# Performance work log

Hardware: AMD Instinct MI355X
Metric: run time of the kernel (lower is better)

## Reference

```python
import jax, jax.numpy as jnp
import numpy as np

B, S, HID = 2, 2048, 5120
H = 32
D_NOPE, D_ROPE, D_V = 128, 64, 128
D_Q = D_NOPE + D_ROPE          # 192, q/k head dim
Q_RANK, KV_RANK = 1536, 512
THETA = 10000.0
EPS = 1e-6


def setup_inputs() -> dict:
    key = jax.random.key(0)
    ks = jax.random.split(key, 8)
    w = lambda k, shape: jax.random.normal(k, shape, jnp.float32) * 0.02
    hidden_states = jax.random.normal(ks[0], (B, S, HID), jnp.float32)
    position_ids = jnp.broadcast_to(jnp.arange(S, dtype=jnp.int32), (B, S))
    attention_mask = jnp.broadcast_to(
        jnp.tril(jnp.ones((S, S), bool))[None, None], (B, 1, S, S))
    return {
        "hidden_states": hidden_states,
        "q_a_proj_w": w(ks[1], (Q_RANK, HID)),
        "q_a_ln_w": jnp.ones((Q_RANK,), jnp.float32),
        "q_b_proj_w": w(ks[2], (H * D_Q, Q_RANK)),
        "kv_a_proj_w": w(ks[3], (KV_RANK + D_ROPE, HID)),
        "kv_a_ln_w": jnp.ones((KV_RANK,), jnp.float32),
        "kv_b_proj_w": w(ks[4], (H * (D_NOPE + D_V), KV_RANK)),
        "o_proj_w": w(ks[5], (HID, H * D_V)),
        "position_ids": position_ids,
        "attention_mask": attention_mask,
    }


def _rms_norm(x, w, eps=EPS):
    x32 = x.astype(jnp.float32)
    var = jnp.mean(x32 * x32, axis=-1, keepdims=True)
    return (x32 * jax.lax.rsqrt(var + eps)).astype(x.dtype) * w


def _deinterleave(x):
    # view(..., d//2, 2).transpose(-1, -2).reshape(..., d)
    return jnp.concatenate([x[..., 0::2], x[..., 1::2]], axis=-1)


def _rotate_half(x):
    h = x.shape[-1] // 2
    return jnp.concatenate([-x[..., h:], x[..., :h]], axis=-1)


def _mla_forward(hidden_states, q_a_proj_w, q_a_ln_w, q_b_proj_w,
                 kv_a_proj_w, kv_a_ln_w, kv_b_proj_w, o_proj_w,
                 position_ids, attention_mask):
    b, s, _ = hidden_states.shape
    # low-rank Q path
    q_c = hidden_states @ q_a_proj_w.T                        # [b,s,Q_RANK]
    q = _rms_norm(q_c, q_a_ln_w) @ q_b_proj_w.T               # [b,s,H*D_Q]
    q = q.reshape(b, s, H, D_Q).transpose(0, 2, 1, 3)         # [b,H,s,D_Q]
    q_nope, q_pe = q[..., :D_NOPE], q[..., D_NOPE:]
    # compressed KV path (MQA rope part shared across heads)
    ckv = hidden_states @ kv_a_proj_w.T                       # [b,s,KV_RANK+D_ROPE]
    compressed, k_pe = ckv[..., :KV_RANK], ckv[..., KV_RANK:]
    k_pe = k_pe.reshape(b, s, 1, D_ROPE).transpose(0, 2, 1, 3)  # [b,1,s,D_ROPE]
    kv = _rms_norm(compressed, kv_a_ln_w) @ kv_b_proj_w.T     # [b,s,H*(D_NOPE+D_V)]
    kv = kv.reshape(b, s, H, D_NOPE + D_V).transpose(0, 2, 1, 3)
    k_nope, v = kv[..., :D_NOPE], kv[..., D_NOPE:]
    # decoupled RoPE (interleaved layout, DeepSeek-V2 style)
    inv_freq = 1.0 / (THETA ** (jnp.arange(0, D_ROPE, 2, dtype=jnp.float32) / D_ROPE))
    t = jnp.arange(s, dtype=jnp.float32)
    emb = jnp.concatenate([t[:, None] * inv_freq, t[:, None] * inv_freq], axis=-1)
    cos = jnp.cos(emb)[position_ids][:, None]                 # [b,1,s,D_ROPE]
    sin = jnp.sin(emb)[position_ids][:, None]
    q_pe = _deinterleave(q_pe)
    k_pe = _deinterleave(k_pe)
    q_pe = q_pe * cos + _rotate_half(q_pe) * sin
    k_pe = k_pe * cos + _rotate_half(k_pe) * sin
    # assemble full q/k and attend
    query = jnp.concatenate([q_nope, q_pe], axis=-1)          # [b,H,s,D_Q]
    key = jnp.concatenate(
        [k_nope, jnp.broadcast_to(k_pe, (b, H, s, D_ROPE))], axis=-1)
    scale = D_Q ** -0.5
    scores = jnp.einsum('bhqd,bhkd->bhqk', query, key) * scale
    scores = jnp.where(attention_mask, scores, jnp.float32(-1e9))
    probs = jax.nn.softmax(scores.astype(jnp.float32), axis=-1).astype(query.dtype)
    attn = jnp.einsum('bhqk,bhkd->bhqd', probs, v)            # [b,H,s,D_V]
    attn = attn.transpose(0, 2, 1, 3).reshape(b, s, H * D_V)
    return attn @ o_proj_w.T                                   # [b,s,HID]


def reference(hidden_states, q_a_proj_w, q_a_ln_w, q_b_proj_w,
              kv_a_proj_w, kv_a_ln_w, kv_b_proj_w, o_proj_w,
              position_ids, attention_mask):
    return _mla_forward(hidden_states, q_a_proj_w, q_a_ln_w, q_b_proj_w,
                        kv_a_proj_w, kv_a_ln_w, kv_b_proj_w, o_proj_w,
                        position_ids, attention_mask)
```

## Files before the change

### kernel.cpp

```cpp
#include <hip/hip_runtime.h>
#include <hip/hip_bf16.h>

typedef __bf16 bf16_t;
typedef __bf16 bf16x4 __attribute__((ext_vector_type(4)));
typedef __bf16 bf16x8 __attribute__((ext_vector_type(8)));
typedef float f32x4 __attribute__((ext_vector_type(4)));

#define B_ 2
#define S_ 2048
#define HID_ 5120
#define H_ 32
#define D_NOPE_ 128
#define D_ROPE_ 64
#define D_V_ 128
#define D_Q_ 192
#define EPS_ 1e-6f

#define GLDS16(g, l)                                                          \
  __builtin_amdgcn_global_load_lds(                                           \
      (const __attribute__((address_space(1))) void*)(g),                     \
      (__attribute__((address_space(3))) void*)(l), 16, 0, 0)

__global__ __launch_bounds__(256) void f32_to_bf16_k(const float* __restrict__ x,
                                                     bf16_t* __restrict__ y, long n) {
  long i = ((long)blockIdx.x * 256 + threadIdx.x) * 8;
  if (i + 8 <= n) {
    float4 f0 = *(const float4*)(x + i);
    float4 f1 = *(const float4*)(x + i + 4);
    bf16x8 o;
    o[0] = (bf16_t)f0.x; o[1] = (bf16_t)f0.y; o[2] = (bf16_t)f0.z; o[3] = (bf16_t)f0.w;
    o[4] = (bf16_t)f1.x; o[5] = (bf16_t)f1.y; o[6] = (bf16_t)f1.z; o[7] = (bf16_t)f1.w;
    *(bf16x8*)(y + i) = o;
  }
}

template <int CMODE>
__global__ __launch_bounds__(256) void gemm128(const bf16_t* __restrict__ A,
                                               const bf16_t* __restrict__ W,
                                               void* __restrict__ Cv,
                                               bf16_t* __restrict__ vTp,
                                               int M, int N, int K) {
  __shared__ bf16_t As[128 * 32];
  __shared__ bf16_t Ws[128 * 32];
  const int tid = threadIdx.x;
  const int lane = tid & 63;
  const int wave = tid >> 6;
  const int bm = blockIdx.y * 128;
  const int bn = blockIdx.x * 128;
  const int wm = (wave >> 1) * 64;
  const int wn = (wave & 1) * 64;
  const int ll = lane & 15;
  const int kg = (lane >> 4) * 8;
  const int r0 = tid >> 2;
  const int cc0 = (tid & 3) * 8;
  const bf16_t* Ag0 = A + (size_t)(bm + r0) * K + cc0;
  const bf16_t* Ag1 = A + (size_t)(bm + 64 + r0) * K + cc0;
  const bf16_t* Wg0 = W + (size_t)(bn + r0) * K + cc0;
  const bf16_t* Wg1 = W + (size_t)(bn + 64 + r0) * K + cc0;
  bf16_t* Al0 = &As[tid * 8];
  bf16_t* Al1 = &As[(tid + 256) * 8];
  bf16_t* Wl0 = &Ws[tid * 8];
  bf16_t* Wl1 = &Ws[(tid + 256) * 8];

  f32x4 acc[4][4];
#pragma unroll
  for (int m = 0; m < 4; m++)
#pragma unroll
    for (int n = 0; n < 4; n++) acc[m][n] = {};

  for (int k0 = 0; k0 < K; k0 += 32) {
    GLDS16(Ag0 + k0, Al0);
    GLDS16(Ag1 + k0, Al1);
    GLDS16(Wg0 + k0, Wl0);
    GLDS16(Wg1 + k0, Wl1);
    __syncthreads();
    bf16x8 af[4], bfr[4];
#pragma unroll
    for (int m = 0; m < 4; m++)
      af[m] = *(const bf16x8*)&As[(wm + m * 16 + ll) * 32 + kg];
#pragma unroll
    for (int n = 0; n < 4; n++)
      bfr[n] = *(const bf16x8*)&Ws[(wn + n * 16 + ll) * 32 + kg];
#pragma unroll
    for (int m = 0; m < 4; m++)
#pragma unroll
      for (int n = 0; n < 4; n++)
        acc[m][n] = __builtin_amdgcn_mfma_f32_16x16x32_bf16(af[m], bfr[n], acc[m][n], 0, 0, 0);
    __syncthreads();
  }

  const int rb = (lane >> 4) * 4;
  if constexpr (CMODE == 2) {
    bf16_t* KN = (bf16_t*)Cv;
#pragma unroll
    for (int m = 0; m < 4; m++)
#pragma unroll
      for (int n = 0; n < 4; n++) {
        int mrow = bm + wm + m * 16 + rb;
        int nn = bn + wn + n * 16 + ll;
        int hh = nn >> 8, cc = nn & 255;
        if (cc < 128) {
          bf16_t* p = KN + ((size_t)mrow * H_ + hh) * 128 + cc;
#pragma unroll
          for (int rr = 0; rr < 4; rr++)
            p[(size_t)rr * (H_ * 128)] = (bf16_t)acc[m][n][rr];
        } else {
          int bb = mrow >> 11;
          int s0 = mrow & 2047;
          bf16x4 o;
          o[0] = (bf16_t)acc[m][n][0]; o[1] = (bf16_t)acc[m][n][1];
          o[2] = (bf16_t)acc[m][n][2]; o[3] = (bf16_t)acc[m][n][3];
          *(bf16x4*)(vTp + (((size_t)bb * H_ + hh) * 128 + (cc - 128)) * S_ + s0) = o;
        }
      }
  } else {
#pragma unroll
    for (int m = 0; m < 4; m++)
#pragma unroll
      for (int n = 0; n < 4; n++) {
        int row = bm + wm + m * 16 + rb;
        int col = bn + wn + n * 16 + ll;
        if (CMODE == 1) {
          float* C = (float*)Cv;
#pragma unroll
          for (int rr = 0; rr < 4; rr++)
            C[(size_t)(row + rr) * N + col] = acc[m][n][rr];
        } else {
          bf16_t* C = (bf16_t*)Cv;
#pragma unroll
          for (int rr = 0; rr < 4; rr++)
            C[(size_t)(row + rr) * N + col] = (bf16_t)acc[m][n][rr];
        }
      }
  }
}

__global__ __launch_bounds__(256) void gemm_bt64(const bf16_t* __restrict__ A,
                                                 const bf16_t* __restrict__ W,
                                                 bf16_t* __restrict__ C,
                                                 int M, int N, int K) {
  __shared__ bf16_t As[64 * 40];
  __shared__ bf16_t Ws[64 * 40];
  const int tid = threadIdx.x;
  const int bm = blockIdx.y * 64;
  const int bn = blockIdx.x * 64;
  const int wave = tid >> 6, lane = tid & 63;
  const int wm = (wave >> 1) * 32, wn = (wave & 1) * 32;
  const int srow = tid >> 2;
  const int scol = (tid & 3) * 8;
  const bf16_t* Ap16 = A + (size_t)(bm + srow) * K + scol;
  const bf16_t* Wp = W + (size_t)(bn + srow) * K + scol;
  f32x4 acc00 = {}, acc01 = {}, acc10 = {}, acc11 = {};
  const int r = lane & 15;
  const int kq = (lane >> 4) * 8;
  for (int k0 = 0; k0 < K; k0 += 32) {
    *(bf16x8*)&As[srow * 40 + scol] = *(const bf16x8*)(Ap16 + k0);
    *(bf16x8*)&Ws[srow * 40 + scol] = *(const bf16x8*)(Wp + k0);
    __syncthreads();
    bf16x8 a0 = *(bf16x8*)&As[(wm + r) * 40 + kq];
    bf16x8 a1 = *(bf16x8*)&As[(wm + 16 + r) * 40 + kq];
    bf16x8 b0 = *(bf16x8*)&Ws[(wn + r) * 40 + kq];
    bf16x8 b1 = *(bf16x8*)&Ws[(wn + 16 + r) * 40 + kq];
    acc00 = __builtin_amdgcn_mfma_f32_16x16x32_bf16(a0, b0, acc00, 0, 0, 0);
    acc01 = __builtin_amdgcn_mfma_f32_16x16x32_bf16(a0, b1, acc01, 0, 0, 0);
    acc10 = __builtin_amdgcn_mfma_f32_16x16x32_bf16(a1, b0, acc10, 0, 0, 0);
    acc11 = __builtin_amdgcn_mfma_f32_16x16x32_bf16(a1, b1, acc11, 0, 0, 0);
    __syncthreads();
  }
  const int col = lane & 15;
  const int rb = (lane >> 4) * 4;
#pragma unroll
  for (int rr = 0; rr < 4; rr++) {
    int m0r = bm + wm + rb + rr;
    int m1r = m0r + 16;
    C[(size_t)m0r * N + (bn + wn + col)]      = (bf16_t)acc00[rr];
    C[(size_t)m0r * N + (bn + wn + 16 + col)] = (bf16_t)acc01[rr];
    C[(size_t)m1r * N + (bn + wn + col)]      = (bf16_t)acc10[rr];
    C[(size_t)m1r * N + (bn + wn + 16 + col)] = (bf16_t)acc11[rr];
  }
}

__global__ __launch_bounds__(256) void rmsnorm_k(const bf16_t* __restrict__ x,
                                                 const float* __restrict__ w,
                                                 bf16_t* __restrict__ y,
                                                 int dim, int xstride) {
  const int row = blockIdx.x;
  const bf16_t* xr = x + (size_t)row * xstride;
  bf16_t* yr = y + (size_t)row * dim;
  float ss = 0.f;
  for (int i = threadIdx.x; i < dim; i += 256) {
    float v = (float)xr[i];
    ss += v * v;
  }
  for (int off = 32; off > 0; off >>= 1) ss += __shfl_down(ss, off);
  __shared__ float red[4];
  __shared__ float s_rinv;
  if ((threadIdx.x & 63) == 0) red[threadIdx.x >> 6] = ss;
  __syncthreads();
  if (threadIdx.x == 0) {
    float tot = red[0] + red[1] + red[2] + red[3];
    s_rinv = 1.0f / sqrtf(tot / (float)dim + EPS_);
  }
  __syncthreads();
  float rinv = s_rinv;
  for (int i = threadIdx.x; i < dim; i += 256)
    yr[i] = (bf16_t)((float)xr[i] * rinv * w[i]);
}

__global__ __launch_bounds__(64) void rope_k(const bf16_t* __restrict__ src,
                                             bf16_t* __restrict__ dst,
                                             const int* __restrict__ pos_ids,
                                             int heads_per_pos, int sstride,
                                             int dstride) {
  __shared__ float xs[64];
  const int rrow = blockIdx.x;
  const int j = threadIdx.x;
  const bf16_t* s = src + (size_t)rrow * sstride;
  xs[j] = (float)s[j];
  __syncthreads();
  const int pos = pos_ids[rrow / heads_per_pos];
  const int i = j & 31;
  float freq = powf(10000.0f, -(float)i / 32.0f);
  float ang = (float)pos * freq;
  float c = cosf(ang), sn = sinf(ang);
  float outv;
  if (j < 32)
    outv = xs[2 * j] * c - xs[2 * j + 1] * sn;
  else
    outv = xs[2 * i + 1] * c + xs[2 * i] * sn;
  dst[(size_t)rrow * dstride + j] = (bf16_t)outv;
}

__global__ __launch_bounds__(256, 2) void flash_attn2(
    const bf16_t* __restrict__ q, const bf16_t* __restrict__ knope,
    const bf16_t* __restrict__ kpe, const bf16_t* __restrict__ vT,
    bf16_t* __restrict__ attn) {
  __shared__ bf16_t KF[12288];
  __shared__ bf16_t VF[8192];
  __shared__ bf16_t PF[8192];
  const int tid = threadIdx.x;
  const int w = tid >> 6;
  const int lane = tid & 63;
  const int ll = lane & 15;
  const int g0 = lane >> 4;
  const int bh = blockIdx.y;
  const int b = bh >> 5;
  const int h = bh & 31;
  const int q0 = ((int)gridDim.x - 1 - (int)blockIdx.x) * 128;
  const int bS = b * S_;
  bf16_t* PFw = PF + w * 2048;

  bf16x8 qf[2][6];
#pragma unroll
  for (int qs = 0; qs < 2; qs++)
#pragma unroll
    for (int ks = 0; ks < 6; ks++)
      qf[qs][ks] = *(const bf16x8*)(
          q + (((size_t)(bS + q0 + 32 * w + 16 * qs + ll)) * H_ + h) * D_Q_ +
          32 * ks + 8 * g0);

  f32x4 acc[2][8];
#pragma unroll
  for (int qs = 0; qs < 2; qs++)
#pragma unroll
    for (int dt = 0; dt < 8; dt++) acc[qs][dt] = {};
  float m_run[2] = {-1e30f, -1e30f};
  float l_run[2] = {0.f, 0.f};

  const bf16_t* kptr[6];
  int kstr[6];
#pragma unroll
  for (int i = 0; i < 6; i++) {
    int c = tid + 256 * i;
    int t_ = c / 384;
    int rem = c - t_ * 384;
    int ks_ = rem >> 6;
    int g_ = (rem >> 4) & 3;
    int ll_ = c & 15;
    int row = 16 * t_ + ll_;
    int k = 32 * ks_ + 8 * g_;
    if (k < 128) {
      kptr[i] = knope + ((size_t)(bS + row) * H_ + h) * 128 + k;
      kstr[i] = H_ * 128;
    } else {
      kptr[i] = kpe + (size_t)(bS + row) * 64 + (k - 128);
      kstr[i] = 64;
    }
  }
  const bf16_t* vptr[4];
#pragma unroll
  for (int i = 0; i < 4; i++) {
    int c = tid + 256 * i;
    int ll_ = c & 15;
    int g_ = (c >> 4) & 3;
    int ks2_ = (c >> 6) & 1;
    int dt_ = c >> 7;
    vptr[i] = vT + (((size_t)b * H_ + h) * 128 + 16 * dt_ + ll_) * S_ +
              32 * ks2_ + 8 * g_;
  }

  bf16x8 kst[6], vst[4];
  auto load_kv = [&]() {
#pragma unroll
    for (int i = 0; i < 6; i++) kst[i] = *(const bf16x8*)kptr[i];
#pragma unroll
    for (int i = 0; i < 4; i++) vst[i] = *(const bf16x8*)vptr[i];
#pragma unroll
    for (int i = 0; i < 6; i++) kptr[i] += (size_t)64 * kstr[i];
#pragma unroll
    for (int i = 0; i < 4; i++) vptr[i] += 64;
  };

  load_kv();
  const int nkt = (q0 >> 6) + 2;
  const float scale = 0.07216878364870322f;

  for (int kt = 0; kt < nkt; kt++) {
    const int k0 = kt * 64;
    __syncthreads();
#pragma unroll
    for (int i = 0; i < 6; i++) *(bf16x8*)&KF[(tid + 256 * i) * 8] = kst[i];
#pragma unroll
    for (int i = 0; i < 4; i++) *(bf16x8*)&VF[(tid + 256 * i) * 8] = vst[i];
    __syncthreads();
    if (kt + 1 < nkt) load_kv();

    f32x4 sv[2][4];
#pragma unroll
    for (int qs = 0; qs < 2; qs++)
#pragma unroll
      for (int t = 0; t < 4; t++) sv[qs][t] = {};
#pragma unroll
    for (int ks = 0; ks < 6; ks++) {
      bf16x8 bq0 = qf[0][ks], bq1 = qf[1][ks];
#pragma unroll
      for (int t = 0; t < 4; t++) {
        bf16x8 ak = *(bf16x8*)&KF[(t * 6 + ks) * 512 + lane * 8];
        sv[0][t] = __builtin_amdgcn_mfma_f32_16x16x32_bf16(ak, bq0, sv[0][t], 0, 0, 0);
        sv[1][t] = __builtin_amdgcn_mfma_f32_16x16x32_bf16(ak, bq1, sv[1][t], 0, 0, 0);
      }
    }

    float alq[2];
#pragma unroll
    for (int qs = 0; qs < 2; qs++) {
      const int qg = q0 + 32 * w + 16 * qs + ll;
      float mx = m_run[qs];
#pragma unroll
      for (int t = 0; t < 4; t++)
#pragma unroll
        for (int r = 0; r < 4; r++) {
          float s = sv[qs][t][r] * scale;
          int kv = k0 + 16 * t + 4 * g0 + r;
          s = (kv > qg) ? -1e30f : s;
          sv[qs][t][r] = s;
          mx = fmaxf(mx, s);
        }
      mx = fmaxf(mx, __shfl_xor(mx, 16));
      mx = fmaxf(mx, __shfl_xor(mx, 32));
      float al = __expf(m_run[qs] - mx);
      float rs = 0.f;
#pragma unroll
      for (int t = 0; t < 4; t++) {
        bf16x4 pv;
#pragma unroll
        for (int r = 0; r < 4; r++) {
          float p = __expf(sv[qs][t][r] - mx);
          rs += p;
          pv[r] = (bf16_t)p;
        }
        int elem = ((qs * 2 + (t >> 1)) * 4 + 2 * (t & 1) + (g0 >> 1)) * 128 +
                   ll * 8 + 4 * (g0 & 1);
        *(bf16x4*)&PFw[elem] = pv;
      }
      rs += __shfl_xor(rs, 16);
      rs += __shfl_xor(rs, 32);
      l_run[qs] = l_run[qs] * al + rs;
      m_run[qs] = mx;
      alq[qs] = al;
    }

#pragma unroll
    for (int qs = 0; qs < 2; qs++)
#pragma unroll
      for (int r = 0; r < 4; r++) {
        float a = __shfl(alq[qs], 4 * g0 + r);
#pragma unroll
        for (int dt = 0; dt < 8; dt++) acc[qs][dt][r] *= a;
      }

#pragma unroll
    for (int ks2 = 0; ks2 < 2; ks2++) {
      bf16x8 ap0 = *(bf16x8*)&PFw[ks2 * 512 + lane * 8];
      bf16x8 ap1 = *(bf16x8*)&PFw[(2 + ks2) * 512 + lane * 8];
#pragma unroll
      for (int dt = 0; dt < 8; dt++) {
        bf16x8 bv = *(bf16x8*)&VF[(dt * 2 + ks2) * 512 + lane * 8];
        acc[0][dt] = __builtin_amdgcn_mfma_f32_16x16x32_bf16(ap0, bv, acc[0][dt], 0, 0, 0);
        acc[1][dt] = __builtin_amdgcn_mfma_f32_16x16x32_bf16(ap1, bv, acc[1][dt], 0, 0, 0);
      }
    }
  }

#pragma unroll
  for (int qs = 0; qs < 2; qs++) {
    float linv = 1.f / l_run[qs];
#pragma unroll
    for (int r = 0; r < 4; r++) {
      float inv = __shfl(linv, 4 * g0 + r);
      int qrow = q0 + 32 * w + 16 * qs + 4 * g0 + r;
      bf16_t* op = attn + (((size_t)(bS + qrow)) * H_ + h) * D_V_ + ll;
#pragma unroll
      for (int dt = 0; dt < 8; dt++)
        op[dt * 16] = (bf16_t)(acc[qs][dt][r] * inv);
    }
  }
}

extern "C" void kernel_launch(void* const* d_in, const int* in_sizes, int n_in,
                              void* d_out, int out_size, void* d_ws, size_t ws_size,
                              hipStream_t stream) {
  const float* hidden  = (const float*)d_in[0];
  const float* q_a_w   = (const float*)d_in[1];
  const float* q_a_ln  = (const float*)d_in[2];
  const float* q_b_w   = (const float*)d_in[3];
  const float* kv_a_w  = (const float*)d_in[4];
  const float* kv_a_ln = (const float*)d_in[5];
  const float* kv_b_w  = (const float*)d_in[6];
  const float* o_w     = (const float*)d_in[7];
  const int*   pos_ids = (const int*)d_in[8];
  float* out = (float*)d_out;
  char* ws = (char*)d_ws;
  const int M = B_ * S_;

  bf16_t* q_ws   = (bf16_t*)(ws + 0);
  bf16_t* knope_ws=(bf16_t*)(ws + 50331648);
  bf16_t* vT_ws  = (bf16_t*)(ws + 83886080);
  bf16_t* kpe_ws = (bf16_t*)(ws + 117440512);
  bf16_t* Wslot  = (bf16_t*)(ws + 117964800);
  bf16_t* qc_ws  = (bf16_t*)(ws + 159907840);
  bf16_t* qcn_ws = (bf16_t*)(ws + 172490752);
  bf16_t* ckv_ws = (bf16_t*)(ws + 185073664);
  bf16_t* ckvn_ws= (bf16_t*)(ws + 189792256);
  bf16_t* attn_ws= (bf16_t*)(ws + 159907840);
  bf16_t* hid_bf = (bf16_t*)(ws + 50331648);

  f32_to_bf16_k<<<(int)((4096L * 5120) / 2048), 256, 0, stream>>>(hidden, hid_bf, 4096L * 5120);
  f32_to_bf16_k<<<1536 * 5120 / 2048, 256, 0, stream>>>(q_a_w, Wslot, 1536L * 5120);
  gemm128<0><<<dim3(1536 / 128, M / 128), 256, 0, stream>>>(hid_bf, Wslot, qc_ws, nullptr, M, 1536, 5120);
  rmsnorm_k<<<M, 256, 0, stream>>>(qc_ws, q_a_ln, qcn_ws, 1536, 1536);
  f32_to_bf16_k<<<576 * 5120 / 2048, 256, 0, stream>>>(kv_a_w, Wslot, 576L * 5120);
  gemm_bt64<<<dim3(576 / 64, M / 64), 256, 0, stream>>>(hid_bf, Wslot, ckv_ws, M, 576, 5120);
  rmsnorm_k<<<M, 256, 0, stream>>>(ckv_ws, kv_a_ln, ckvn_ws, 512, 576);
  f32_to_bf16_k<<<6144 * 1536 / 2048, 256, 0, stream>>>(q_b_w, Wslot, 6144L * 1536);
  gemm128<0><<<dim3(6144 / 128, M / 128), 256, 0, stream>>>(qcn_ws, Wslot, q_ws, nullptr, M, 6144, 1536);
  f32_to_bf16_k<<<8192 * 512 / 2048, 256, 0, stream>>>(kv_b_w, Wslot, 8192L * 512);
  gemm128<2><<<dim3(8192 / 128, M / 128), 256, 0, stream>>>(ckvn_ws, Wslot, knope_ws, vT_ws, M, 8192, 512);
  rope_k<<<M * H_, 64, 0, stream>>>(q_ws + 128, q_ws + 128, pos_ids, H_, D_Q_, D_Q_);
  rope_k<<<M, 64, 0, stream>>>(ckv_ws + 512, kpe_ws, pos_ids, 1, 576, 64);
  flash_attn2<<<dim3(S_ / 128, B_ * H_), 256, 0, stream>>>(q_ws, knope_ws, kpe_ws, vT_ws, attn_ws);
  f32_to_bf16_k<<<5120 * 4096 / 2048, 256, 0, stream>>>(o_w, Wslot, 5120L * 4096);
  gemm128<1><<<dim3(5120 / 128, M / 128), 256, 0, stream>>>(attn_ws, Wslot, out, nullptr, M, 5120, 4096);
}
```

Baseline: 1.281 ms.

## Restructure flash attention to 512 threads with one 16-row Q tile per wave

The attention kernel moves from 4 waves each handling 32 query rows to 8 waves each handling 16 rows. This halves per-wave register state (accumulators, Q fragments, staging) to raise occupancy and spreads the K/V loads over more threads. It also folds the softmax scale and log2e into Q so exp2 can be used, skips the causal mask on tiles that are fully below the diagonal, and raises wave priority around the MFMA loops. The rope kernel swaps powf/cosf/sinf for exp2f and the fast __sincosf, which trades some accuracy at large angles for cheaper math. Rounding the pre-scaled Q to bf16 adds a little extra rounding error.

```diff
diff --git a/kernel.cpp b/kernel.cpp
--- a/kernel.cpp
+++ b/kernel.cpp
@@ -220,9 +220,10 @@
   __syncthreads();
   const int pos = pos_ids[rrow / heads_per_pos];
   const int i = j & 31;
-  float freq = powf(10000.0f, -(float)i / 32.0f);
+  float freq = exp2f(-(float)i * 0.4152410118609203f);
   float ang = (float)pos * freq;
-  float c = cosf(ang), sn = sinf(ang);
+  float c, sn;
+  __sincosf(ang, &sn, &c);
   float outv;
   if (j < 32)
     outv = xs[2 * j] * c - xs[2 * j + 1] * sn;
@@ -231,7 +232,7 @@
   dst[(size_t)rrow * dstride + j] = (bf16_t)outv;
 }
 
-__global__ __launch_bounds__(256, 2) void flash_attn2(
+__global__ __launch_bounds__(512, 4) void flash_attn3(
     const bf16_t* __restrict__ q, const bf16_t* __restrict__ knope,
     const bf16_t* __restrict__ kpe, const bf16_t* __restrict__ vT,
     bf16_t* __restrict__ attn) {
@@ -248,30 +249,30 @@
   const int h = bh & 31;
   const int q0 = ((int)gridDim.x - 1 - (int)blockIdx.x) * 128;
   const int bS = b * S_;
-  bf16_t* PFw = PF + w * 2048;
-
-  bf16x8 qf[2][6];
-#pragma unroll
-  for (int qs = 0; qs < 2; qs++)
-#pragma unroll
-    for (int ks = 0; ks < 6; ks++)
-      qf[qs][ks] = *(const bf16x8*)(
-          q + (((size_t)(bS + q0 + 32 * w + 16 * qs + ll)) * H_ + h) * D_Q_ +
-          32 * ks + 8 * g0);
-
-  f32x4 acc[2][8];
-#pragma unroll
-  for (int qs = 0; qs < 2; qs++)
-#pragma unroll
-    for (int dt = 0; dt < 8; dt++) acc[qs][dt] = {};
-  float m_run[2] = {-1e30f, -1e30f};
-  float l_run[2] = {0.f, 0.f};
-
-  const bf16_t* kptr[6];
-  int kstr[6];
-#pragma unroll
-  for (int i = 0; i < 6; i++) {
-    int c = tid + 256 * i;
+  bf16_t* PFw = PF + w * 1024;
+
+  const float qsc = 0.07216878364870322f * 1.4426950408889634f;
+  bf16x8 qf[6];
+#pragma unroll
+  for (int ks = 0; ks < 6; ks++) {
+    bf16x8 raw = *(const bf16x8*)(
+        q + (((size_t)(bS + q0 + 16 * w + ll)) * H_ + h) * D_Q_ + 32 * ks + 8 * g0);
+    bf16x8 sc;
+#pragma unroll
+    for (int j = 0; j < 8; j++) sc[j] = (bf16_t)((float)raw[j] * qsc);
+    qf[ks] = sc;
+  }
+
+  f32x4 acc[8];
+#pragma unroll
+  for (int dt = 0; dt < 8; dt++) acc[dt] = {};
+  float m_run = -1e30f, l_run = 0.f;
+
+  const bf16_t* kptr[3];
+  int kstr[3];
+#pragma unroll
+  for (int i = 0; i < 3; i++) {
+    int c = tid + 512 * i;
     int t_ = c / 384;
     int rem = c - t_ * 384;
     int ks_ = rem >> 6;
@@ -287,10 +288,10 @@
       kstr[i] = 64;
     }
   }
-  const bf16_t* vptr[4];
-#pragma unroll
-  for (int i = 0; i < 4; i++) {
-    int c = tid + 256 * i;
+  const bf16_t* vptr[2];
+#pragma unroll
+  for (int i = 0; i < 2; i++) {
+    int c = tid + 512 * i;
     int ll_ = c & 15;
     int g_ = (c >> 4) & 3;
     int ks2_ = (c >> 6) & 1;
@@ -299,121 +300,114 @@
               32 * ks2_ + 8 * g_;
   }
 
-  bf16x8 kst[6], vst[4];
+  bf16x8 kst[3], vst[2];
   auto load_kv = [&]() {
 #pragma unroll
-    for (int i = 0; i < 6; i++) kst[i] = *(const bf16x8*)kptr[i];
-#pragma unroll
-    for (int i = 0; i < 4; i++) vst[i] = *(const bf16x8*)vptr[i];
-#pragma unroll
-    for (int i = 0; i < 6; i++) kptr[i] += (size_t)64 * kstr[i];
-#pragma unroll
-    for (int i = 0; i < 4; i++) vptr[i] += 64;
+    for (int i = 0; i < 3; i++) kst[i] = *(const bf16x8*)kptr[i];
+#pragma unroll
+    for (int i = 0; i < 2; i++) vst[i] = *(const bf16x8*)vptr[i];
+#pragma unroll
+    for (int i = 0; i < 3; i++) kptr[i] += (size_t)64 * kstr[i];
+#pragma unroll
+    for (int i = 0; i < 2; i++) vptr[i] += 64;
   };
 
   load_kv();
   const int nkt = (q0 >> 6) + 2;
-  const float scale = 0.07216878364870322f;
 
   for (int kt = 0; kt < nkt; kt++) {
     const int k0 = kt * 64;
     __syncthreads();
 #pragma unroll
-    for (int i = 0; i < 6; i++) *(bf16x8*)&KF[(tid + 256 * i) * 8] = kst[i];
-#pragma unroll
-    for (int i = 0; i < 4; i++) *(bf16x8*)&VF[(tid + 256 * i) * 8] = vst[i];
+    for (int i = 0; i < 3; i++) *(bf16x8*)&KF[(tid + 512 * i) * 8] = kst[i];
+#pragma unroll
+    for (int i = 0; i < 2; i++) *(bf16x8*)&VF[(tid + 512 * i) * 8] = vst[i];
     __syncthreads();
     if (kt + 1 < nkt) load_kv();
 
-    f32x4 sv[2][4];
-#pragma unroll
-    for (int qs = 0; qs < 2; qs++)
-#pragma unroll
-      for (int t = 0; t < 4; t++) sv[qs][t] = {};
+    f32x4 sv[4];
+#pragma unroll
+    for (int t = 0; t < 4; t++) sv[t] = {};
+    __builtin_amdgcn_s_setprio(1);
 #pragma unroll
     for (int ks = 0; ks < 6; ks++) {
-      bf16x8 bq0 = qf[0][ks], bq1 = qf[1][ks];
+      bf16x8 bq = qf[ks];
 #pragma unroll
       for (int t = 0; t < 4; t++) {
         bf16x8 ak = *(bf16x8*)&KF[(t * 6 + ks) * 512 + lane * 8];
-        sv[0][t] = __builtin_amdgcn_mfma_f32_16x16x32_bf16(ak, bq0, sv[0][t], 0, 0, 0);
-        sv[1][t] = __builtin_amdgcn_mfma_f32_16x16x32_bf16(ak, bq1, sv[1][t], 0, 0, 0);
+        sv[t] = __builtin_amdgcn_mfma_f32_16x16x32_bf16(ak, bq, sv[t], 0, 0, 0);
       }
     }
-
-    float alq[2];
-#pragma unroll
-    for (int qs = 0; qs < 2; qs++) {
-      const int qg = q0 + 32 * w + 16 * qs + ll;
-      float mx = m_run[qs];
+    __builtin_amdgcn_s_setprio(0);
+
+    const int qg = q0 + 16 * w + ll;
+    float mx = m_run;
+    if (k0 + 63 > q0 + 16 * w) {
 #pragma unroll
       for (int t = 0; t < 4; t++)
 #pragma unroll
         for (int r = 0; r < 4; r++) {
-          float s = sv[qs][t][r] * scale;
-          int kv = k0 + 16 * t + 4 * g0 + r;
-          s = (kv > qg) ? -1e30f : s;
-          sv[qs][t][r] = s;
+          float s = sv[t][r];
+          s = (k0 + 16 * t + 4 * g0 + r > qg) ? -1e30f : s;
+          sv[t][r] = s;
           mx = fmaxf(mx, s);
         }
-      mx = fmaxf(mx, __shfl_xor(mx, 16));
-      mx = fmaxf(mx, __shfl_xor(mx, 32));
-      float al = __expf(m_run[qs] - mx);
-      float rs = 0.f;
-#pragma unroll
-      for (int t = 0; t < 4; t++) {
-        bf16x4 pv;
-#pragma unroll
-        for (int r = 0; r < 4; r++) {
-          float p = __expf(sv[qs][t][r] - mx);
-          rs += p;
-          pv[r] = (bf16_t)p;
-        }
-        int elem = ((qs * 2 + (t >> 1)) * 4 + 2 * (t & 1) + (g0 >> 1)) * 128 +
-                   ll * 8 + 4 * (g0 & 1);
-        *(bf16x4*)&PFw[elem] = pv;
+    } else {
+#pragma unroll
+      for (int t = 0; t < 4; t++)
+#pragma unroll
+        for (int r = 0; r < 4; r++) mx = fmaxf(mx, sv[t][r]);
+    }
+    mx = fmaxf(mx, __shfl_xor(mx, 16));
+    mx = fmaxf(mx, __shfl_xor(mx, 32));
+    float al = exp2f(m_run - mx);
+    float rs = 0.f;
+#pragma unroll
+    for (int t = 0; t < 4; t++) {
+      bf16x4 pv;
+#pragma unroll
+      for (int r = 0; r < 4; r++) {
+        float p = exp2f(sv[t][r] - mx);
+        rs += p;
+        pv[r] = (bf16_t)p;
       }
-      rs += __shfl_xor(rs, 16);
-      rs += __shfl_xor(rs, 32);
-      l_run[qs] = l_run[qs] * al + rs;
-      m_run[qs] = mx;
-      alq[qs] = al;
-    }
-
-#pragma unroll
-    for (int qs = 0; qs < 2; qs++)
-#pragma unroll
-      for (int r = 0; r < 4; r++) {
-        float a = __shfl(alq[qs], 4 * g0 + r);
-#pragma unroll
-        for (int dt = 0; dt < 8; dt++) acc[qs][dt][r] *= a;
-      }
-
+      int elem = ((t >> 1) * 4 + 2 * (t & 1) + (g0 >> 1)) * 128 + ll * 8 + 4 * (g0 & 1);
+      *(bf16x4*)&PFw[elem] = pv;
+    }
+    rs += __shfl_xor(rs, 16);
+    rs += __shfl_xor(rs, 32);
+    l_run = l_run * al + rs;
+    m_run = mx;
+
+#pragma unroll
+    for (int r = 0; r < 4; r++) {
+      float a = __shfl(al, 4 * g0 + r);
+#pragma unroll
+      for (int dt = 0; dt < 8; dt++) acc[dt][r] *= a;
+    }
+
+    __builtin_amdgcn_s_setprio(1);
 #pragma unroll
     for (int ks2 = 0; ks2 < 2; ks2++) {
-      bf16x8 ap0 = *(bf16x8*)&PFw[ks2 * 512 + lane * 8];
-      bf16x8 ap1 = *(bf16x8*)&PFw[(2 + ks2) * 512 + lane * 8];
+      bf16x8 ap = *(bf16x8*)&PFw[ks2 * 512 + lane * 8];
 #pragma unroll
       for (int dt = 0; dt < 8; dt++) {
         bf16x8 bv = *(bf16x8*)&VF[(dt * 2 + ks2) * 512 + lane * 8];
-        acc[0][dt] = __builtin_amdgcn_mfma_f32_16x16x32_bf16(ap0, bv, acc[0][dt], 0, 0, 0);
-        acc[1][dt] = __builtin_amdgcn_mfma_f32_16x16x32_bf16(ap1, bv, acc[1][dt], 0, 0, 0);
+        acc[dt] = __builtin_amdgcn_mfma_f32_16x16x32_bf16(ap, bv, acc[dt], 0, 0, 0);
       }
     }
-  }
-
-#pragma unroll
-  for (int qs = 0; qs < 2; qs++) {
-    float linv = 1.f / l_run[qs];
-#pragma unroll
-    for (int r = 0; r < 4; r++) {
-      float inv = __shfl(linv, 4 * g0 + r);
-      int qrow = q0 + 32 * w + 16 * qs + 4 * g0 + r;
-      bf16_t* op = attn + (((size_t)(bS + qrow)) * H_ + h) * D_V_ + ll;
-#pragma unroll
-      for (int dt = 0; dt < 8; dt++)
-        op[dt * 16] = (bf16_t)(acc[qs][dt][r] * inv);
-    }
+    __builtin_amdgcn_s_setprio(0);
+  }
+
+  float linv = 1.f / l_run;
+#pragma unroll
+  for (int r = 0; r < 4; r++) {
+    float inv = __shfl(linv, 4 * g0 + r);
+    int qrow = q0 + 16 * w + 4 * g0 + r;
+    bf16_t* op = attn + (((size_t)(bS + qrow)) * H_ + h) * D_V_ + ll;
+#pragma unroll
+    for (int dt = 0; dt < 8; dt++)
+      op[dt * 16] = (bf16_t)(acc[dt][r] * inv);
   }
 }
 
@@ -458,7 +452,7 @@
   gemm128<2><<<dim3(8192 / 128, M / 128), 256, 0, stream>>>(ckvn_ws, Wslot, knope_ws, vT_ws, M, 8192, 512);
   rope_k<<<M * H_, 64, 0, stream>>>(q_ws + 128, q_ws + 128, pos_ids, H_, D_Q_, D_Q_);
   rope_k<<<M, 64, 0, stream>>>(ckv_ws + 512, kpe_ws, pos_ids, 1, 576, 64);
-  flash_attn2<<<dim3(S_ / 128, B_ * H_), 256, 0, stream>>>(q_ws, knope_ws, kpe_ws, vT_ws, attn_ws);
+  flash_attn3<<<dim3(S_ / 128, B_ * H_), 512, 0, stream>>>(q_ws, knope_ws, kpe_ws, vT_ws, attn_ws);
   f32_to_bf16_k<<<5120 * 4096 / 2048, 256, 0, stream>>>(o_w, Wslot, 5120L * 4096);
   gemm128<1><<<dim3(5120 / 128, M / 128), 256, 0, stream>>>(attn_ws, Wslot, out, nullptr, M, 5120, 4096);
 }
```

Result: faster. 1.239 ms (-3.3%).
